# Performance work log

Hardware: AMD Instinct MI355X
Metric: run time of the kernel (lower is better)

The kernel has to match this reference:

```python
import jax, jax.numpy as jnp
import numpy as np

K = 3  # kernel_size

def _extract_patches(x):
    # x: (b, n, h, w) -> (b, n, K*K, h, w), stride=1, padding=1 (zeros), row-major kernel order like nn.Unfold
    b, n, h, w = x.shape
    xp = jnp.pad(x, ((0, 0), (0, 0), (1, 1), (1, 1)))
    slices = [xp[:, :, i:i + h, j:j + w] for i in range(K) for j in range(K)]
    return jnp.stack(slices, axis=2)

def _conv3x3(x, w, b):
    # x: (b, cin, h, w), w: (cout, cin, 3, 3)
    y = jax.lax.conv_general_dilated(
        x, w, window_strides=(1, 1), padding=((1, 1), (1, 1)),
        dimension_numbers=('NCHW', 'OIHW', 'NCHW'))
    return y + b[None, :, None, None]

def setup_inputs() -> dict:
    key = jax.random.key(0)
    ks = jax.random.split(key, 6)
    b, n, h, w = 8, 256, 64, 64
    cout, r = 256, 4
    cm = n // r
    s = lambda fan: 1.0 / np.sqrt(fan)
    return {
        'x':    jax.random.normal(ks[0], (b, n, h, w), jnp.float32),
        'w_c1': jax.random.normal(ks[1], (cm, n), jnp.float32) * s(n),
        'b_c1': jnp.zeros((cm,), jnp.float32),
        'w_c2': jax.random.normal(ks[2], (n, cm), jnp.float32) * s(cm),
        'b_c2': jnp.zeros((n,), jnp.float32),
        'w_d1': jax.random.normal(ks[3], (cm, n, 3, 3), jnp.float32) * s(n * 9),
        'b_d1': jnp.zeros((cm,), jnp.float32),
        'w_d2': jax.random.normal(ks[4], (K * K, cm), jnp.float32) * s(cm),
        'b_d2': jnp.zeros((K * K,), jnp.float32),
        'W':    jax.random.normal(ks[5], (cout, n, K * K), jnp.float32) * s(n * K * K),
    }

def reference(x, w_c1, b_c1, w_c2, b_c2, w_d1, b_d1, w_d2, b_d2, W):
    # channel attention branch: 1x1 -> ReLU -> 1x1, output (b, n, h, w)
    yc = jax.nn.relu(jnp.einsum('bnhw,mn->bmhw', x, w_c1) + b_c1[None, :, None, None])
    c = jnp.einsum('bmhw,nm->bnhw', yc, w_c2) + b_c2[None, :, None, None]
    # kernel (spatial) attention branch: 3x3 -> ReLU -> 1x1, output (b, K*K, h, w)
    yd = jax.nn.relu(_conv3x3(x, w_d1, b_d1))
    d = jnp.einsum('bmhw,km->bkhw', yd, w_d2) + b_d2[None, :, None, None]
    # unfold and modulate: (b, n, K*K, h, w)
    patches = _extract_patches(x)
    attn = 1.0 + jnp.tanh(d[:, None, :, :, :] + c[:, :, None, :, :])
    # conv3d with (out, in, K*K, 1, 1) weight == per-pixel contraction over (n, K*K)
    out = jnp.einsum('bnkhw,onk->bohw', patches * attn, W)
    return out
```

## Files before the change

### kernel.cpp

```cpp
#include <hip/hip_runtime.h>
#include <hip/hip_bf16.h>
#include <stdint.h>

typedef __attribute__((ext_vector_type(8))) short bf16x8;
typedef __attribute__((ext_vector_type(4))) short bf16x4;
typedef __attribute__((ext_vector_type(4))) float f32x4;
typedef __attribute__((ext_vector_type(4))) int   i32x4;
typedef __attribute__((ext_vector_type(2))) int   i32x2;

#define DEV static __device__ __forceinline__

DEV float bf2f(short s) {
    unsigned u = ((unsigned)(unsigned short)s) << 16;
    return __builtin_bit_cast(float, u);
}
DEV short f2bf(float f) {
    unsigned u = __builtin_bit_cast(unsigned, f);
    unsigned r = u + 0x7fffu + ((u >> 16) & 1u);
    return (short)(r >> 16);
}
DEV unsigned cvt_pk_bf16(float lo, float hi) {
    unsigned r;
    asm("v_cvt_pk_bf16_f32 %0, %1, %2" : "=v"(r) : "v"(lo), "v"(hi));
    return r;
}
DEV void async_copy16(void* lds, const void* g) {
    __builtin_amdgcn_global_load_lds((const __attribute__((address_space(1))) void*)g,
                                     (__attribute__((address_space(3))) void*)lds, 16, 0, 0);
}

#define PTOT 32768
#define NEXP2 (-2.885390081777927f)

#define WS_WC1F 0
#define WS_WC2F 32768
#define WS_WD1F 65536
#define WS_WF   360448
#define WS_EKT  1540096
#define WS_EN   2719744
#define WS_XT   19496960

__global__ __launch_bounds__(256) void k_prep(const float* __restrict__ W, const float* __restrict__ w_d1,
                                              const float* __restrict__ w_c1, const float* __restrict__ w_c2,
                                              short* __restrict__ Wf, short* __restrict__ wd1f,
                                              short* __restrict__ wc1f, short* __restrict__ wc2f) {
    int t = blockIdx.x * 256 + threadIdx.x;
    if (t < 589824) {
        int i = t & 7, lane = (t >> 3) & 63, ot = (t >> 9) & 15, kt = t >> 13;
        int o = ot * 16 + (lane & 15);
        int n = (kt & 7) * 32 + (lane >> 4) * 8 + i;
        Wf[t] = f2bf(2.0f * W[o * 2304 + n * 9 + (kt >> 3)]);
    } else if (t < 589824 + 147456) {
        int t2 = t - 589824;
        int i = t2 & 7, lane = (t2 >> 3) & 63, wv = (t2 >> 9) & 3, kc = t2 >> 11;
        int m = wv * 16 + (lane & 15);
        int n = (kc & 7) * 32 + (lane >> 4) * 8 + i;
        wd1f[t2] = f2bf(w_d1[m * 2304 + n * 9 + (kc >> 3)]);
    } else if (t < 589824 + 147456 + 16384) {
        int t3 = t - (589824 + 147456);
        int i = t3 & 7, lane = (t3 >> 3) & 63, wv = (t3 >> 9) & 3, s = t3 >> 11;
        int m = wv * 16 + (lane & 15);
        int n = s * 32 + (lane >> 4) * 8 + i;
        wc1f[t3] = f2bf(w_c1[m * 256 + n]);
    } else if (t < 589824 + 147456 + 32768) {
        int t4 = t - (589824 + 147456 + 16384);
        int i = t4 & 7, lane = (t4 >> 3) & 63, ot = (t4 >> 9) & 15, s = t4 >> 13;
        int o = ot * 16 + (lane & 15);
        int kk = s * 32 + (lane >> 4) * 8 + i;
        wc2f[t4] = f2bf(w_c2[o * 64 + kk]);
    }
}

__global__ __launch_bounds__(256) void k_prep_xt(const float* __restrict__ x, short* __restrict__ xT8) {
    __shared__ short t[64 * 74];
    const int rw = ((blockIdx.x & 7) << 6) + (blockIdx.x >> 3);
    const int b = rw >> 6, hr = rw & 63;
    const int tid = threadIdx.x;
    const int hp = hr + 1;
    #define XI(HP, NP, WP) ((((size_t)(b) * 66 + (HP)) * 32 + (NP)) * 66 + (WP)) * 8
    if (tid < 64) {
        int np = tid & 31, wp = (tid & 32) ? 65 : 0;
        *(i32x4*)(xT8 + XI(hp, np, wp)) = i32x4{0, 0, 0, 0};
    }
    if (hr == 0) {
        for (int i = tid; i < 2 * 32 * 66; i += 256) {
            int pl = (i >= 32 * 66) ? 65 : 0;
            int rem = (i >= 32 * 66) ? i - 32 * 66 : i;
            int np = rem / 66, wp = rem - np * 66;
            *(i32x4*)(xT8 + XI(pl, np, wp)) = i32x4{0, 0, 0, 0};
        }
    }
    const int dn = tid >> 6, w = tid & 63;
    for (int p = 0; p < 4; ++p) {
        __syncthreads();
        #pragma unroll
        for (int jj = 0; jj < 16; ++jj) {
            int n = p * 64 + dn * 16 + jj;
            t[w * 74 + dn * 16 + jj] = f2bf(x[(((size_t)(b * 256 + n) * 64) + hr) * 64 + w]);
        }
        __syncthreads();
        #pragma unroll
        for (int q = 0; q < 2; ++q) {
            int nl = q * 4 + dn;
            *(bf16x8*)(xT8 + XI(hp, p * 8 + nl, w + 1)) = *(const bf16x8*)(t + w * 74 + nl * 8);
        }
    }
    #undef XI
}

#define BR_YD_OFF  9216
#define BR_ENT_OFF (BR_YD_OFF + 17152)
#define BR_TOTAL   (BR_ENT_OFF + 33792)

__global__ __launch_bounds__(512, 4) void k_branch(const short* __restrict__ xT8,
        const float* __restrict__ b_c1, const float* __restrict__ b_c2,
        const float* __restrict__ b_d1, const float* __restrict__ w_d2, const float* __restrict__ b_d2,
        const short* __restrict__ wc1f, const short* __restrict__ wc2f, const short* __restrict__ wd1f,
        short* __restrict__ enF, float* __restrict__ ekT) {
    extern __shared__ char smem[];
    short* yc  = (short*)smem;
    float* ydl = (float*)(smem + BR_YD_OFF);
    short* ent = (short*)(smem + BR_ENT_OFF);

    const int rw = ((blockIdx.x & 7) << 6) + (blockIdx.x >> 3);
    const int b = rw >> 6, h = rw & 63;
    const int p0 = rw << 6;
    const int tid = threadIdx.x;
    const int lane = tid & 63, wave = tid >> 6;
    const int l16 = lane & 15, lg = lane >> 4;
    const int wn = wave & 3, wm = wave >> 2;
    const int cm = wn * 16 + l16;
    const size_t b66h = (size_t)(b * 66 + h);
    const int wcol = wm * 32 + l16;

    #define CONV_A(DST, KC) {                                                           \
        int k9_ = (KC) >> 3;                                                            \
        int kh_ = (k9_ * 11) >> 5, kw_ = k9_ - 3 * kh_;                                 \
        const short* xa_ = xT8 + (((b66h + kh_) * 32 + ((KC) & 7) * 4 + lg) * 66        \
                                  + wcol + kw_) * 8;                                    \
        DST[0] = *(const bf16x8*)(xa_);                                                 \
        DST[1] = *(const bf16x8*)(xa_ + 128);                                           \
    }

    {
        f32x4 acc[2] = {};
        const short* wp_ = wc1f + wn * 512 + lane * 8;
        const short* xg1 = xT8 + (((b66h + 1) * 32 + lg) * 66 + wcol + 1) * 8;
        bf16x8 bcur = *(const bf16x8*)(wp_);
        bf16x8 a0 = *(const bf16x8*)(xg1), a1 = *(const bf16x8*)(xg1 + 128);
        #pragma unroll
        for (int s = 0; s < 8; ++s) {
            bf16x8 bc = bcur, c0 = a0, c1 = a1;
            if (s < 7) {
                bcur = *(const bf16x8*)(wp_ + (s + 1) * 2048);
                a0 = *(const bf16x8*)(xg1 + (s + 1) * 2112);
                a1 = *(const bf16x8*)(xg1 + (s + 1) * 2112 + 128);
            }
            acc[0] = __builtin_amdgcn_mfma_f32_16x16x32_bf16(c0, bc, acc[0], 0, 0, 0);
            acc[1] = __builtin_amdgcn_mfma_f32_16x16x32_bf16(c1, bc, acc[1], 0, 0, 0);
        }
        float bias = b_c1[cm];
        #pragma unroll
        for (int mt = 0; mt < 2; ++mt)
            #pragma unroll
            for (int r = 0; r < 4; ++r) {
                int px = wm * 32 + mt * 16 + lg * 4 + r;
                float v = acc[mt][r] + bias;
                yc[px * 72 + cm] = f2bf(v > 0.f ? v : 0.f);
            }
    }

    {
        f32x4 acc[2] = {};
        const short* wp_ = wd1f + wn * 512 + lane * 8;
        bf16x8 b0 = *(const bf16x8*)(wp_);
        bf16x8 b1 = *(const bf16x8*)(wp_ + 2048);
        bf16x8 b2 = *(const bf16x8*)(wp_ + 4096);
        bf16x8 aA[2], aB[2], aC[2];
        CONV_A(aA, 0) CONV_A(aB, 1) CONV_A(aC, 2)
        for (int kc = 0; kc < 72; kc += 3) {
            {
                bf16x8 c0 = aA[0], c1 = aA[1], bc = b0;
                int cn = (kc + 3 < 72) ? kc + 3 : 71;
                CONV_A(aA, cn)
                b0 = *(const bf16x8*)(wp_ + cn * 2048);
                acc[0] = __builtin_amdgcn_mfma_f32_16x16x32_bf16(c0, bc, acc[0], 0, 0, 0);
                acc[1] = __builtin_amdgcn_mfma_f32_16x16x32_bf16(c1, bc, acc[1], 0, 0, 0);
            }
            {
                bf16x8 c0 = aB[0], c1 = aB[1], bc = b1;
                int cn = (kc + 4 < 72) ? kc + 4 : 71;
                CONV_A(aB, cn)
                b1 = *(const bf16x8*)(wp_ + cn * 2048);
                acc[0] = __builtin_amdgcn_mfma_f32_16x16x32_bf16(c0, bc, acc[0], 0, 0, 0);
                acc[1] = __builtin_amdgcn_mfma_f32_16x16x32_bf16(c1, bc, acc[1], 0, 0, 0);
            }
            {
                bf16x8 c0 = aC[0], c1 = aC[1], bc = b2;
                int cn = (kc + 5 < 72) ? kc + 5 : 71;
                CONV_A(aC, cn)
                b2 = *(const bf16x8*)(wp_ + cn * 2048);
                acc[0] = __builtin_amdgcn_mfma_f32_16x16x32_bf16(c0, bc, acc[0], 0, 0, 0);
                acc[1] = __builtin_amdgcn_mfma_f32_16x16x32_bf16(c1, bc, acc[1], 0, 0, 0);
            }
        }
        float bias = b_d1[cm];
        #pragma unroll
        for (int mt = 0; mt < 2; ++mt)
            #pragma unroll
            for (int r = 0; r < 4; ++r) {
                int px = wm * 32 + mt * 16 + lg * 4 + r;
                float v = acc[mt][r] + bias;
                ydl[px * 67 + cm] = v > 0.f ? v : 0.f;
            }
    }
    #undef CONV_A
    __syncthreads();

    {
        f32x4 acc[2][4] = {};
        #pragma unroll
        for (int s = 0; s < 2; ++s) {
            int k0 = s * 32;
            bf16x8 afr[2], bfr[4];
            #pragma unroll
            for (int mt = 0; mt < 2; ++mt)
                afr[mt] = *(const bf16x8*)(yc + (wm * 32 + mt * 16 + l16) * 72 + k0 + lg * 8);
            #pragma unroll
            for (int nt = 0; nt < 4; ++nt)
                bfr[nt] = *(const bf16x8*)(wc2f + s * 8192 + (wn * 4 + nt) * 512 + lane * 8);
            #pragma unroll
            for (int mt = 0; mt < 2; ++mt)
                #pragma unroll
                for (int nt = 0; nt < 4; ++nt)
                    acc[mt][nt] = __builtin_amdgcn_mfma_f32_16x16x32_bf16(afr[mt], bfr[nt], acc[mt][nt], 0, 0, 0);
        }
        #pragma unroll
        for (int nt = 0; nt < 4; ++nt) {
            int nc = wn * 64 + nt * 16 + l16;
            float bias = b_c2[nc];
            #pragma unroll
            for (int mt = 0; mt < 2; ++mt)
                #pragma unroll
                for (int r = 0; r < 4; ++r) {
                    int px = wm * 32 + mt * 16 + lg * 4 + r;
                    float cv = acc[mt][nt][r] + bias;
                    ent[px * 264 + nc] = f2bf(exp2f(NEXP2 * cv));
                }
        }
    }

    for (int t = tid; t < 576; t += 512) {
        int k = t >> 6, px = t & 63;
        float sum = b_d2[k];
        const float* yr = ydl + px * 67;
        const float* wr = w_d2 + k * 64;
        #pragma unroll 8
        for (int m = 0; m < 64; ++m) sum += yr[m] * wr[m];
        ekT[(size_t)k * PTOT + p0 + px] = exp2f(NEXP2 * sum);
    }
    __syncthreads();

    for (int i = tid; i < 2048; i += 512) {
        int px = i & 63, seg = i >> 6;
        *(bf16x8*)(enF + (size_t)p0 * 256 + (seg >> 2) * 2048 + (seg & 3) * 512 + px * 8)
            = *(const bf16x8*)(ent + px * 264 + seg * 8);
    }
}

#define FN4_Z1    4096
#define FN4_B0    8192
#define FN4_B1    24576
#define FN4_EKL   40960
#define FN4_TOTAL 43264

__global__ __launch_bounds__(512, 4) void k_final(const short* __restrict__ xT8,
        const short* __restrict__ Wf, const short* __restrict__ enF, const float* __restrict__ ekT,
        float* __restrict__ out) {
    extern __shared__ char smem[];
    short* z0  = (short*)smem;
    short* z1  = (short*)(smem + FN4_Z1);
    short* Bl0 = (short*)(smem + FN4_B0);
    short* Bl1 = (short*)(smem + FN4_B1);
    float* ekl = (float*)(smem + FN4_EKL);

    const int rw = ((blockIdx.x & 7) << 6) + (blockIdx.x >> 3);
    const int b = rw >> 6, h = rw & 63;
    const int p0 = rw << 6;
    const int tid = threadIdx.x;
    const int lane = tid & 63, wave = tid >> 6;
    const int l16 = lane & 15, lg = lane >> 4;

    for (int i = tid; i < 576; i += 512)
        ekl[i] = ekT[(size_t)(i >> 6) * PTOT + p0 + (i & 63)];

    const size_t b66h = (size_t)(b * 66 + h);
    const int zpx = lane;
    const int wh = wave >> 1, wl = wave & 1;
    const short* xb0 = xT8 + (b66h * 32 + wh) * 528 + zpx * 8 + wl * 4;
    bf16x4 e_regs[8];
    {
        const short* enb = enF + (size_t)p0 * 256 + wh * 512 + zpx * 8 + wl * 4;
        #pragma unroll
        for (int c8 = 0; c8 < 8; ++c8) e_regs[c8] = *(const bf16x4*)(enb + c8 * 2048);
    }
    const int zwoff = (zpx >> 4) * 512 + ((zpx & 15) + wh * 16) * 8 + wl * 4;
    const char* WfB = (const char*)Wf;

    #define DMA_B(KC, BUF) {                                                            \
        _Pragma("unroll")                                                               \
        for (int c = 0; c < 2; ++c) {                                                   \
            const char* g_ = WfB + (size_t)(KC) * 16384 + (wave * 2 + c) * 1024 + lane * 16; \
            async_copy16((char*)(BUF) + (wave * 2 + c) * 1024, g_);                     \
        }                                                                               \
    }
    bf16x4 xr;
    #define XLOAD(KC2) {                                                                \
        int k3_ = (KC2) >> 3, c8_ = (KC2) & 7;                                          \
        int kh_ = (k3_ * 11) >> 5, kw_ = k3_ - 3 * kh_;                                 \
        xr = *(const bf16x4*)(xb0 + kh_ * 16896 + c8_ * 2112 + kw_ * 8);                \
    }
    #define ZBUILD(ZBUF, EKROW, EIDX) {                                                 \
        bf16x4 er = e_regs[EIDX];                                                       \
        float ekv = ekl[(EKROW) * 64 + zpx];                                            \
        float q0 = __builtin_fmaf(ekv, bf2f(er[0]), 1.0f);                              \
        float q1 = __builtin_fmaf(ekv, bf2f(er[1]), 1.0f);                              \
        float q2 = __builtin_fmaf(ekv, bf2f(er[2]), 1.0f);                              \
        float q3 = __builtin_fmaf(ekv, bf2f(er[3]), 1.0f);                              \
        i32x2 zz;                                                                       \
        zz[0] = cvt_pk_bf16(bf2f(xr[0]) * __builtin_amdgcn_rcpf(q0),                    \
                            bf2f(xr[1]) * __builtin_amdgcn_rcpf(q1));                   \
        zz[1] = cvt_pk_bf16(bf2f(xr[2]) * __builtin_amdgcn_rcpf(q2),                    \
                            bf2f(xr[3]) * __builtin_amdgcn_rcpf(q3));                   \
        *(i32x2*)((ZBUF) + zwoff) = zz;                                                 \
    }

    DMA_B(0, Bl0)
    XLOAD(0)
    __syncthreads();
    ZBUILD(z0, 0, 0)
    XLOAD(1)
    __syncthreads();

    f32x4 acc[4][2] = {};

    #define STEP(C8, P1, P2, EKROW) {                                                   \
        short* zcur = ((C8) & 1) ? z1 : z0;                                             \
        short* znxt = ((C8) & 1) ? z0 : z1;                                             \
        short* bcur = ((C8) & 1) ? Bl1 : Bl0;                                           \
        short* bnxt = ((C8) & 1) ? Bl0 : Bl1;                                           \
        if (P1) {                                                                       \
            DMA_B(k3 * 8 + (C8) + 1, bnxt)                                              \
            ZBUILD(znxt, EKROW, ((C8) + 1) & 7)                                         \
        }                                                                               \
        if (P2) XLOAD(k3 * 8 + (C8) + 2)                                                \
        bf16x8 afr[4], bfr[2];                                                          \
        _Pragma("unroll")                                                               \
        for (int mt = 0; mt < 4; ++mt)                                                  \
            afr[mt] = *(const bf16x8*)(zcur + mt * 512 + lane * 8);                     \
        bfr[0] = *(const bf16x8*)(bcur + (wave * 2 + 0) * 512 + lane * 8);              \
        bfr[1] = *(const bf16x8*)(bcur + (wave * 2 + 1) * 512 + lane * 8);              \
        __builtin_amdgcn_s_setprio(1);                                                  \
        _Pragma("unroll")                                                               \
        for (int mt = 0; mt < 4; ++mt) {                                                \
            acc[mt][0] = __builtin_amdgcn_mfma_f32_16x16x32_bf16(afr[mt], bfr[0], acc[mt][0], 0, 0, 0); \
            acc[mt][1] = __builtin_amdgcn_mfma_f32_16x16x32_bf16(afr[mt], bfr[1], acc[mt][1], 0, 0, 0); \
        }                                                                               \
        __builtin_amdgcn_s_setprio(0);                                                  \
        __syncthreads();                                                                \
    }

    for (int k3 = 0; k3 < 8; ++k3) {
        STEP(0, 1, 1, k3) STEP(1, 1, 1, k3) STEP(2, 1, 1, k3) STEP(3, 1, 1, k3)
        STEP(4, 1, 1, k3) STEP(5, 1, 1, k3) STEP(6, 1, 1, k3) STEP(7, 1, 1, k3 + 1)
    }
    {
        const int k3 = 8;
        STEP(0, 1, 1, k3) STEP(1, 1, 1, k3) STEP(2, 1, 1, k3) STEP(3, 1, 1, k3)
        STEP(4, 1, 1, k3) STEP(5, 1, 1, k3) STEP(6, 1, 0, k3) STEP(7, 0, 0, k3)
    }
    #undef STEP
    #undef ZBUILD
    #undef XLOAD
    #undef DMA_B

    #pragma unroll
    for (int mt = 0; mt < 4; ++mt)
        #pragma unroll
        for (int nt = 0; nt < 2; ++nt) {
            int o = wave * 32 + nt * 16 + l16;
            float* d = out + (((size_t)b * 256 + o) * 64 + h) * 64 + mt * 16 + lg * 4;
            *(f32x4*)d = acc[mt][nt];
        }
}

extern "C" void kernel_launch(void* const* d_in, const int* in_sizes, int n_in,
                              void* d_out, int out_size, void* d_ws, size_t ws_size,
                              hipStream_t stream) {
    const float* x    = (const float*)d_in[0];
    const float* w_c1 = (const float*)d_in[1];
    const float* b_c1 = (const float*)d_in[2];
    const float* w_c2 = (const float*)d_in[3];
    const float* b_c2 = (const float*)d_in[4];
    const float* w_d1 = (const float*)d_in[5];
    const float* b_d1 = (const float*)d_in[6];
    const float* w_d2 = (const float*)d_in[7];
    const float* b_d2 = (const float*)d_in[8];
    const float* Wt   = (const float*)d_in[9];
    float* out = (float*)d_out;
    char* ws = (char*)d_ws;

    short* wc1f = (short*)(ws + WS_WC1F);
    short* wc2f = (short*)(ws + WS_WC2F);
    short* wd1f = (short*)(ws + WS_WD1F);
    short* Wf   = (short*)(ws + WS_WF);
    float* ekT  = (float*)(ws + WS_EKT);
    short* enF  = (short*)(ws + WS_EN);
    short* xT8  = (short*)(ws + WS_XT);

    (void)hipFuncSetAttribute((const void*)k_branch, hipFuncAttributeMaxDynamicSharedMemorySize, BR_TOTAL);
    (void)hipFuncSetAttribute((const void*)k_final,  hipFuncAttributeMaxDynamicSharedMemorySize, FN4_TOTAL);

    k_prep<<<3008, 256, 0, stream>>>(Wt, w_d1, w_c1, w_c2, Wf, wd1f, wc1f, wc2f);
    k_prep_xt<<<512, 256, 0, stream>>>(x, xT8);
    k_branch<<<512, 512, BR_TOTAL, stream>>>(xT8, b_c1, b_c2, b_d1, w_d2, b_d2, wc1f, wc2f, wd1f, enF, ekT);
    k_final<<<512, 512, FN4_TOTAL, stream>>>(xT8, Wf, enF, ekT, out);
}
```

Before: 112.3 us.

## Load final-GEMM weights directly into registers and merge prep kernels

In k_final, the LDS double buffer for the weight (B) fragments filled by global_load_lds DMA is removed. Each wave now loads its own B fragments straight from global memory into registers, prefetching two steps ahead with even/odd register sets. This cuts LDS use from about 43KB to about 10KB per block and removes the LDS round trip, at the cost of more VGPRs and exposed global latency. Separately, the two prep kernels are merged into one launch, with block ranges selecting the weight-repack or x-transpose work, which saves one kernel launch.

```diff
diff --git a/kernel.cpp b/kernel.cpp
--- a/kernel.cpp
+++ b/kernel.cpp
@@ -23,10 +23,6 @@
     unsigned r;
     asm("v_cvt_pk_bf16_f32 %0, %1, %2" : "=v"(r) : "v"(lo), "v"(hi));
     return r;
-}
-DEV void async_copy16(void* lds, const void* g) {
-    __builtin_amdgcn_global_load_lds((const __attribute__((address_space(1))) void*)g,
-                                     (__attribute__((address_space(3))) void*)lds, 16, 0, 0);
 }
 
 #define PTOT 32768
@@ -40,42 +36,45 @@
 #define WS_EN   2719744
 #define WS_XT   19496960
 
-__global__ __launch_bounds__(256) void k_prep(const float* __restrict__ W, const float* __restrict__ w_d1,
+__global__ __launch_bounds__(256) void k_prep_all(const float* __restrict__ W, const float* __restrict__ w_d1,
                                               const float* __restrict__ w_c1, const float* __restrict__ w_c2,
+                                              const float* __restrict__ x,
                                               short* __restrict__ Wf, short* __restrict__ wd1f,
-                                              short* __restrict__ wc1f, short* __restrict__ wc2f) {
-    int t = blockIdx.x * 256 + threadIdx.x;
-    if (t < 589824) {
-        int i = t & 7, lane = (t >> 3) & 63, ot = (t >> 9) & 15, kt = t >> 13;
-        int o = ot * 16 + (lane & 15);
-        int n = (kt & 7) * 32 + (lane >> 4) * 8 + i;
-        Wf[t] = f2bf(2.0f * W[o * 2304 + n * 9 + (kt >> 3)]);
-    } else if (t < 589824 + 147456) {
-        int t2 = t - 589824;
-        int i = t2 & 7, lane = (t2 >> 3) & 63, wv = (t2 >> 9) & 3, kc = t2 >> 11;
-        int m = wv * 16 + (lane & 15);
-        int n = (kc & 7) * 32 + (lane >> 4) * 8 + i;
-        wd1f[t2] = f2bf(w_d1[m * 2304 + n * 9 + (kc >> 3)]);
-    } else if (t < 589824 + 147456 + 16384) {
-        int t3 = t - (589824 + 147456);
-        int i = t3 & 7, lane = (t3 >> 3) & 63, wv = (t3 >> 9) & 3, s = t3 >> 11;
-        int m = wv * 16 + (lane & 15);
-        int n = s * 32 + (lane >> 4) * 8 + i;
-        wc1f[t3] = f2bf(w_c1[m * 256 + n]);
-    } else if (t < 589824 + 147456 + 32768) {
-        int t4 = t - (589824 + 147456 + 16384);
-        int i = t4 & 7, lane = (t4 >> 3) & 63, ot = (t4 >> 9) & 15, s = t4 >> 13;
-        int o = ot * 16 + (lane & 15);
-        int kk = s * 32 + (lane >> 4) * 8 + i;
-        wc2f[t4] = f2bf(w_c2[o * 64 + kk]);
-    }
-}
-
-__global__ __launch_bounds__(256) void k_prep_xt(const float* __restrict__ x, short* __restrict__ xT8) {
+                                              short* __restrict__ wc1f, short* __restrict__ wc2f,
+                                              short* __restrict__ xT8) {
     __shared__ short t[64 * 74];
-    const int rw = ((blockIdx.x & 7) << 6) + (blockIdx.x >> 3);
+    const int tid = threadIdx.x;
+    if (blockIdx.x < 3008) {
+        int tt = blockIdx.x * 256 + tid;
+        if (tt < 589824) {
+            int i = tt & 7, lane = (tt >> 3) & 63, ot = (tt >> 9) & 15, kt = tt >> 13;
+            int o = ot * 16 + (lane & 15);
+            int n = (kt & 7) * 32 + (lane >> 4) * 8 + i;
+            Wf[tt] = f2bf(2.0f * W[o * 2304 + n * 9 + (kt >> 3)]);
+        } else if (tt < 589824 + 147456) {
+            int t2 = tt - 589824;
+            int i = t2 & 7, lane = (t2 >> 3) & 63, wv = (t2 >> 9) & 3, kc = t2 >> 11;
+            int m = wv * 16 + (lane & 15);
+            int n = (kc & 7) * 32 + (lane >> 4) * 8 + i;
+            wd1f[t2] = f2bf(w_d1[m * 2304 + n * 9 + (kc >> 3)]);
+        } else if (tt < 589824 + 147456 + 16384) {
+            int t3 = tt - (589824 + 147456);
+            int i = t3 & 7, lane = (t3 >> 3) & 63, wv = (t3 >> 9) & 3, s = t3 >> 11;
+            int m = wv * 16 + (lane & 15);
+            int n = s * 32 + (lane >> 4) * 8 + i;
+            wc1f[t3] = f2bf(w_c1[m * 256 + n]);
+        } else if (tt < 589824 + 147456 + 32768) {
+            int t4 = tt - (589824 + 147456 + 16384);
+            int i = t4 & 7, lane = (t4 >> 3) & 63, ot = (t4 >> 9) & 15, s = t4 >> 13;
+            int o = ot * 16 + (lane & 15);
+            int kk = s * 32 + (lane >> 4) * 8 + i;
+            wc2f[t4] = f2bf(w_c2[o * 64 + kk]);
+        }
+        return;
+    }
+    const int bid = blockIdx.x - 3008;
+    const int rw = ((bid & 7) << 6) + (bid >> 3);
     const int b = rw >> 6, hr = rw & 63;
-    const int tid = threadIdx.x;
     const int hp = hr + 1;
     #define XI(HP, NP, WP) ((((size_t)(b) * 66 + (HP)) * 32 + (NP)) * 66 + (WP)) * 8
     if (tid < 64) {
@@ -268,21 +267,17 @@
     }
 }
 
-#define FN4_Z1    4096
-#define FN4_B0    8192
-#define FN4_B1    24576
-#define FN4_EKL   40960
-#define FN4_TOTAL 43264
+#define FN5_Z1    4096
+#define FN5_EKL   8192
+#define FN5_TOTAL 10496
 
 __global__ __launch_bounds__(512, 4) void k_final(const short* __restrict__ xT8,
         const short* __restrict__ Wf, const short* __restrict__ enF, const float* __restrict__ ekT,
         float* __restrict__ out) {
     extern __shared__ char smem[];
     short* z0  = (short*)smem;
-    short* z1  = (short*)(smem + FN4_Z1);
-    short* Bl0 = (short*)(smem + FN4_B0);
-    short* Bl1 = (short*)(smem + FN4_B1);
-    float* ekl = (float*)(smem + FN4_EKL);
+    short* z1  = (short*)(smem + FN5_Z1);
+    float* ekl = (float*)(smem + FN5_EKL);
 
     const int rw = ((blockIdx.x & 7) << 6) + (blockIdx.x >> 3);
     const int b = rw >> 6, h = rw & 63;
@@ -305,15 +300,9 @@
         for (int c8 = 0; c8 < 8; ++c8) e_regs[c8] = *(const bf16x4*)(enb + c8 * 2048);
     }
     const int zwoff = (zpx >> 4) * 512 + ((zpx & 15) + wh * 16) * 8 + wl * 4;
-    const char* WfB = (const char*)Wf;
-
-    #define DMA_B(KC, BUF) {                                                            \
-        _Pragma("unroll")                                                               \
-        for (int c = 0; c < 2; ++c) {                                                   \
-            const char* g_ = WfB + (size_t)(KC) * 16384 + (wave * 2 + c) * 1024 + lane * 16; \
-            async_copy16((char*)(BUF) + (wave * 2 + c) * 1024, g_);                     \
-        }                                                                               \
-    }
+    const short* wb0 = Wf + (wave * 2 + 0) * 512 + lane * 8;
+    const short* wb1 = Wf + (wave * 2 + 1) * 512 + lane * 8;
+
     bf16x4 xr;
     #define XLOAD(KC2) {                                                                \
         int k3_ = (KC2) >> 3, c8_ = (KC2) & 7;                                          \
@@ -335,7 +324,9 @@
         *(i32x2*)((ZBUF) + zwoff) = zz;                                                 \
     }
 
-    DMA_B(0, Bl0)
+    bf16x8 Be[2], Bo[2];
+    Be[0] = *(const bf16x8*)(wb0);          Be[1] = *(const bf16x8*)(wb1);
+    Bo[0] = *(const bf16x8*)(wb0 + 8192);   Bo[1] = *(const bf16x8*)(wb1 + 8192);
     XLOAD(0)
     __syncthreads();
     ZBUILD(z0, 0, 0)
@@ -347,24 +338,26 @@
     #define STEP(C8, P1, P2, EKROW) {                                                   \
         short* zcur = ((C8) & 1) ? z1 : z0;                                             \
         short* znxt = ((C8) & 1) ? z0 : z1;                                             \
-        short* bcur = ((C8) & 1) ? Bl1 : Bl0;                                           \
-        short* bnxt = ((C8) & 1) ? Bl0 : Bl1;                                           \
-        if (P1) {                                                                       \
-            DMA_B(k3 * 8 + (C8) + 1, bnxt)                                              \
-            ZBUILD(znxt, EKROW, ((C8) + 1) & 7)                                         \
+        bf16x8 bc0, bc1;                                                                \
+        if ((C8) & 1) { bc0 = Bo[0]; bc1 = Bo[1]; } else { bc0 = Be[0]; bc1 = Be[1]; }  \
+        if (P2) {    \
+            int kb2_ = (k3 * 8 + (C8) + 2) * 8192;                                      \
+            if ((C8) & 1) { Bo[0] = *(const bf16x8*)(wb0 + kb2_);                       \
+                            Bo[1] = *(const bf16x8*)(wb1 + kb2_); }                     \
+            else          { Be[0] = *(const bf16x8*)(wb0 + kb2_);                       \
+                            Be[1] = *(const bf16x8*)(wb1 + kb2_); }                     \
         }                                                                               \
+        if (P1) ZBUILD(znxt, EKROW, ((C8) + 1) & 7)                                     \
         if (P2) XLOAD(k3 * 8 + (C8) + 2)                                                \
-        bf16x8 afr[4], bfr[2];                                                          \
+        bf16x8 afr[4];                                                                  \
         _Pragma("unroll")                                                               \
         for (int mt = 0; mt < 4; ++mt)                                                  \
             afr[mt] = *(const bf16x8*)(zcur + mt * 512 + lane * 8);                     \
-        bfr[0] = *(const bf16x8*)(bcur + (wave * 2 + 0) * 512 + lane * 8);              \
-        bfr[1] = *(const bf16x8*)(bcur + (wave * 2 + 1) * 512 + lane * 8);              \
         __builtin_amdgcn_s_setprio(1);                                                  \
         _Pragma("unroll")                                                               \
         for (int mt = 0; mt < 4; ++mt) {                                                \
-            acc[mt][0] = __builtin_amdgcn_mfma_f32_16x16x32_bf16(afr[mt], bfr[0], acc[mt][0], 0, 0, 0); \
-            acc[mt][1] = __builtin_amdgcn_mfma_f32_16x16x32_bf16(afr[mt], bfr[1], acc[mt][1], 0, 0, 0); \
+            acc[mt][0] = __builtin_amdgcn_mfma_f32_16x16x32_bf16(afr[mt], bc0, acc[mt][0], 0, 0, 0); \
+            acc[mt][1] = __builtin_amdgcn_mfma_f32_16x16x32_bf16(afr[mt], bc1, acc[mt][1], 0, 0, 0); \
         }                                                                               \
         __builtin_amdgcn_s_setprio(0);                                                  \
         __syncthreads();                                                                \
@@ -382,7 +375,6 @@
     #undef STEP
     #undef ZBUILD
     #undef XLOAD
-    #undef DMA_B
 
     #pragma unroll
     for (int mt = 0; mt < 4; ++mt)
@@ -419,10 +411,9 @@
     short* xT8  = (short*)(ws + WS_XT);
 
     (void)hipFuncSetAttribute((const void*)k_branch, hipFuncAttributeMaxDynamicSharedMemorySize, BR_TOTAL);
-    (void)hipFuncSetAttribute((const void*)k_final,  hipFuncAttributeMaxDynamicSharedMemorySize, FN4_TOTAL);
-
-    k_prep<<<3008, 256, 0, stream>>>(Wt, w_d1, w_c1, w_c2, Wf, wd1f, wc1f, wc2f);
-    k_prep_xt<<<512, 256, 0, stream>>>(x, xT8);
+    (void)hipFuncSetAttribute((const void*)k_final,  hipFuncAttributeMaxDynamicSharedMemorySize, FN5_TOTAL);
+
+    k_prep_all<<<3520, 256, 0, stream>>>(Wt, w_d1, w_c1, w_c2, x, Wf, wd1f, wc1f, wc2f, xT8);
     k_branch<<<512, 512, BR_TOTAL, stream>>>(xT8, b_c1, b_c2, b_d1, w_d2, b_d2, wc1f, wc2f, wd1f, enF, ekT);
-    k_final<<<512, 512, FN4_TOTAL, stream>>>(xT8, Wf, enF, ekT, out);
-}
+    k_final<<<512, 512, FN5_TOTAL, stream>>>(xT8, Wf, enF, ekT, out);
+}
```

New measurement: 106.8 us. -4.9%, faster.
